# Kernel optimization log

Measured on AMD Instinct MI355X. Metric: run time of the kernel, lower is better.

Reference implementation:

```python
import jax, jax.numpy as jnp
import numpy as np

B, BAG, H, C = 512, 32, 1024, 53
EPS = 1e-8  # torch F.cosine_similarity denominator clamp


def setup_inputs() -> dict:
    key = jax.random.key(0)
    ks = jax.random.split(key, 5)
    return {
        "sent_reps": jax.random.normal(ks[0], (B, BAG, H), jnp.float32),
        "aug_sent_reps": jax.random.normal(ks[1], (B, BAG, H), jnp.float32),
        "rel_table": jax.random.normal(ks[2], (C, H), jnp.float32),
        "cls_w": jax.random.normal(ks[3], (C, H), jnp.float32) * 0.02,
        "cls_b": jnp.zeros((C,), jnp.float32),
        "labels": jax.random.randint(ks[4], (B,), 0, C),
        "temperature": jnp.asarray(0.1, jnp.float32),
    }


def _cl(rep, aug, bag_rep, T):
    # rep, aug: (B, bag, H); bag_rep: (B, H)
    nr = jnp.linalg.norm(rep, axis=-1)        # (B, bag)
    na = jnp.linalg.norm(aug, axis=-1)        # (B, bag)
    nb = jnp.linalg.norm(bag_rep, axis=-1)    # (B,)
    pos_sim = jnp.sum(rep * aug, axis=-1) / jnp.maximum(nr * na, EPS)  # (B, bag)
    pos = jnp.exp(pos_sim / T)
    # pair[c, j, b] = cos(rep[b, j], bag_rep[c])  -- matches torch permute/broadcast chain
    dots = jnp.einsum('bjh,ch->cjb', rep, bag_rep)               # (B, bag, B)
    denom = jnp.maximum(nb[:, None, None] * nr.T[None], EPS)      # (B, bag, B)
    pair = dots / denom
    idx = jnp.arange(rep.shape[0])
    axis_sim = pair[idx, :, idx]                                  # (B, bag): cos(rep[b,j], bag_rep[b])
    neg = jnp.exp(pair / T).sum(axis=2) - jnp.exp(axis_sim / T)   # (B, bag)
    return jnp.mean(-jnp.log(pos / (pos + neg)))


def reference(sent_reps, aug_sent_reps, rel_table, cls_w, cls_b, labels, temperature):
    # Selective attention per bag (scope slices are uniform bags of size BAG -> vectorized)
    rel = rel_table[labels]                                        # (B, H)
    scale = jnp.sqrt(jnp.asarray(H, sent_reps.dtype))
    scores = jnp.einsum('bh,bjh->bj', rel, sent_reps) / scale      # (B, bag)
    alphas = jax.nn.softmax(scores, axis=-1)
    bag_reps = jnp.einsum('bj,bjh->bh', alphas, sent_reps)         # (B, H)
    bag_out = bag_reps @ cls_w.T + cls_b                           # (B, C)  (dropout in eval = identity)
    cl_loss = _cl(sent_reps, aug_sent_reps, bag_reps, temperature)
    return bag_out, cl_loss
```

## Files before the change

kernel.cpp:

```cpp
#include <hip/hip_runtime.h>
#include <hip/hip_bf16.h>


typedef __bf16 bf16x8 __attribute__((ext_vector_type(8)));
typedef float  f32x4  __attribute__((ext_vector_type(4)));

__device__ inline float wsum(float v) {
    #pragma unroll
    for (int off = 32; off > 0; off >>= 1) v += __shfl_xor(v, off, 64);
    return v;
}

__device__ inline void gll16(const void* g, void* l) {
    __builtin_amdgcn_global_load_lds((const __attribute__((address_space(1))) void*)g,
                                     (__attribute__((address_space(3))) void*)l, 16, 0, 0);
}

__global__ __launch_bounds__(256) void k0_cvt(const float* __restrict__ w, __bf16* __restrict__ wb)
{
    int i = blockIdx.x * 256 + threadIdx.x;
    wb[i] = (i < 53 * 1024) ? (__bf16)w[i] : (__bf16)0.0f;
}

__global__ __launch_bounds__(1024) void k1_bag(
    const float* __restrict__ sent, const float* __restrict__ rel_table,
    const int* __restrict__ labels, float* __restrict__ bag,
    __bf16* __restrict__ bagb, float* __restrict__ nb)
{
    const int b = blockIdx.x, t = threadIdx.x;
    const int lane = t & 63, wave = t >> 6;
    __shared__ float red[32 * 16];
    __shared__ float alphas[32];
    __shared__ float r2[16];

    const float relh = rel_table[(size_t)labels[b] * 1024 + t];
    const float* s = sent + (size_t)b * 32 * 1024;
    float v[32];
    #pragma unroll
    for (int j = 0; j < 32; j++) v[j] = s[j * 1024 + t];

    #pragma unroll
    for (int j = 0; j < 32; j++) {
        float p = wsum(relh * v[j]);
        if (lane == 0) red[j * 16 + wave] = p;
    }
    __syncthreads();

    if (wave == 0) {
        float sj = 0.0f;
        if (lane < 32) {
            #pragma unroll
            for (int w = 0; w < 16; w++) sj += red[lane * 16 + w];
            sj *= (1.0f / 32.0f);
        }
        float m = sj;
        #pragma unroll
        for (int off = 16; off > 0; off >>= 1) m = fmaxf(m, __shfl_xor(m, off, 32));
        float e = __expf(sj - m);
        float sum = e;
        #pragma unroll
        for (int off = 16; off > 0; off >>= 1) sum += __shfl_xor(sum, off, 32);
        if (lane < 32) alphas[lane] = e / sum;
    }
    __syncthreads();

    float bg = 0.0f;
    #pragma unroll
    for (int j = 0; j < 32; j++) bg += alphas[j] * v[j];
    bag[(size_t)b * 1024 + t] = bg;
    bagb[(size_t)b * 1024 + t] = (__bf16)bg;

    float q = wsum(bg * bg);
    if (lane == 0) r2[wave] = q;
    __syncthreads();
    if (t == 0) {
        float s2 = 0.0f;
        #pragma unroll
        for (int w = 0; w < 16; w++) s2 += r2[w];
        nb[b] = sqrtf(s2);
    }
}

__global__ __launch_bounds__(256) void k2_norms(
    const float* __restrict__ sent, const float* __restrict__ aug,
    __bf16* __restrict__ repb, float* __restrict__ nr, float* __restrict__ pos_sim)
{
    const int r = blockIdx.x;
    const int t = threadIdx.x;
    const float* rp = sent + (size_t)r * 1024;
    const float* ap = aug + (size_t)r * 1024;
    float sr = 0.f, sa = 0.f, sd = 0.f;
    #pragma unroll
    for (int i = 0; i < 4; i++) {
        int h = t + i * 256;
        float x = rp[h], y = ap[h];
        sr += x * x; sa += y * y; sd += x * y;
        repb[(size_t)r * 1024 + h] = (__bf16)x;
    }
    sr = wsum(sr); sa = wsum(sa); sd = wsum(sd);
    __shared__ float red[4 * 3];
    const int lane = t & 63, wave = t >> 6;
    if (lane == 0) { red[wave * 3] = sr; red[wave * 3 + 1] = sa; red[wave * 3 + 2] = sd; }
    __syncthreads();
    if (t == 0) {
        float S = 0.f, A = 0.f, D = 0.f;
        #pragma unroll
        for (int w = 0; w < 4; w++) { S += red[w * 3]; A += red[w * 3 + 1]; D += red[w * 3 + 2]; }
        float nrv = sqrtf(S), nav = sqrtf(A);
        nr[r] = nrv;
        pos_sim[r] = D / fmaxf(nrv * nav, 1e-8f);
    }
}

__global__ __launch_bounds__(256) void k3m(
    const __bf16* __restrict__ bagb, const __bf16* __restrict__ cwb,
    const float* __restrict__ bias, float* __restrict__ out)
{
    __shared__ __align__(16) __bf16 Al[64 * 40];
    __shared__ __align__(16) __bf16 Bl[64 * 40];
    const int r0 = blockIdx.x * 64;
    const int t = threadIdx.x, lane = t & 63, w = t >> 6;
    const int m = lane & 15, quad = lane >> 4;
    f32x4 acc[4] = {};
    const int lrow = t >> 2, lk = (t & 3) * 8;

    for (int k0 = 0; k0 < 1024; k0 += 32) {
        __syncthreads();
        *(f32x4*)(&Al[lrow * 40 + lk]) = *(const f32x4*)(&bagb[(size_t)(r0 + lrow) * 1024 + k0 + lk]);
        *(f32x4*)(&Bl[lrow * 40 + lk]) = *(const f32x4*)(&cwb[(size_t)lrow * 1024 + k0 + lk]);
        __syncthreads();
        bf16x8 a = *(const bf16x8*)(&Al[(w * 16 + m) * 40 + quad * 8]);
        #pragma unroll
        for (int n = 0; n < 4; n++) {
            bf16x8 bf = *(const bf16x8*)(&Bl[(n * 16 + m) * 40 + quad * 8]);
            acc[n] = __builtin_amdgcn_mfma_f32_16x16x32_bf16(a, bf, acc[n], 0, 0, 0);
        }
    }
    #pragma unroll
    for (int n = 0; n < 4; n++) {
        const int c = n * 16 + m;
        if (c < 53) {
            #pragma unroll
            for (int i = 0; i < 4; i++) {
                const int r = r0 + w * 16 + quad * 4 + i;
                out[(size_t)r * 53 + c] = acc[n][i] + bias[c];
            }
        }
    }
}

__global__ __launch_bounds__(256) void k4_gemm(
    const __bf16* __restrict__ repb, const __bf16* __restrict__ bagb,
    const float* __restrict__ nr, const float* __restrict__ nb,
    const float* __restrict__ temp, float* __restrict__ E)
{
    __shared__ __align__(16) __bf16 Al[128 * 32];
    __shared__ __align__(16) __bf16 Bl[128 * 32];
    const int cb = blockIdx.x, rb = blockIdx.y;
    const int r0 = rb * 128, c0 = cb * 128;
    const int t = threadIdx.x, lane = t & 63, w = t >> 6;
    const int m = lane & 15, quad = lane >> 4;
    const int wr0 = (w & 1) * 64, wc0 = (w >> 1) * 64;

    f32x4 acc[4][4] = {};

    const int i0 = t * 8, i1 = 2048 + t * 8;
    const int row0 = i0 >> 5, kk0 = i0 & 31;
    const int row1 = i1 >> 5, kk1 = i1 & 31;
    const __bf16* gA0 = repb + (size_t)(r0 + row0) * 1024 + kk0;
    const __bf16* gA1 = repb + (size_t)(r0 + row1) * 1024 + kk1;
    const __bf16* gB0 = bagb + (size_t)(c0 + row0) * 1024 + kk0;
    const __bf16* gB1 = bagb + (size_t)(c0 + row1) * 1024 + kk1;

    for (int k0 = 0; k0 < 1024; k0 += 32) {
        __syncthreads();
        gll16(gA0 + k0, Al + i0);
        gll16(gA1 + k0, Al + i1);
        gll16(gB0 + k0, Bl + i0);
        gll16(gB1 + k0, Bl + i1);
        __syncthreads();
        bf16x8 a[4], bf[4];
        #pragma unroll
        for (int i = 0; i < 4; i++) a[i]  = *(const bf16x8*)(&Al[(wr0 + i * 16 + m) * 32 + quad * 8]);
        #pragma unroll
        for (int n = 0; n < 4; n++) bf[n] = *(const bf16x8*)(&Bl[(wc0 + n * 16 + m) * 32 + quad * 8]);
        #pragma unroll
        for (int i = 0; i < 4; i++)
            #pragma unroll
            for (int n = 0; n < 4; n++)
                acc[i][n] = __builtin_amdgcn_mfma_f32_16x16x32_bf16(a[i], bf[n], acc[i][n], 0, 0, 0);
    }

    const float invT = 1.0f / *temp;
    float nrv[16];
    #pragma unroll
    for (int i = 0; i < 4; i++)
        #pragma unroll
        for (int g = 0; g < 4; g++)
            nrv[i * 4 + g] = nr[r0 + wr0 + i * 16 + quad * 4 + g];
    #pragma unroll
    for (int n = 0; n < 4; n++) {
        const int c = c0 + wc0 + n * 16 + m;
        const float nbv = nb[c];
        #pragma unroll
        for (int i = 0; i < 4; i++) {
            #pragma unroll
            for (int g = 0; g < 4; g++) {
                const int r = r0 + wr0 + i * 16 + quad * 4 + g;
                float pair = acc[i][n][g] / fmaxf(nbv * nrv[i * 4 + g], 1e-8f);
                E[(size_t)r * 512 + c] = __expf(pair * invT);
            }
        }
    }
}

__global__ __launch_bounds__(256) void k5_neg(
    const float* __restrict__ E, const float* __restrict__ pos_sim,
    const float* __restrict__ temp, float* __restrict__ bsums)
{
    const int ct = blockIdx.x & 7, j = blockIdx.x >> 3;
    const int t = threadIdx.x, lane = t & 63, w = t >> 6;
    const int c = ct * 64 + lane;
    __shared__ float red[4][64];

    float s = 0.f;
    const float* base = E + (size_t)j * 512 + c;
    #pragma unroll 8
    for (int b = w * 128; b < w * 128 + 128; b++)
        s += base[(size_t)b * 32 * 512];
    red[w][lane] = s;
    __syncthreads();

    if (t < 64) {
        const int cc = ct * 64 + t;
        float S = red[0][t] + red[1][t] + red[2][t] + red[3][t];
        S -= E[(size_t)((cc << 5) + j) * 512 + cc];
        const float invT = 1.0f / *temp;
        const float lp = pos_sim[(cc << 5) + j] * invT;
        float term = logf(__expf(lp) + S) - lp;
        term = wsum(term);
        if (t == 0) bsums[blockIdx.x] = term;
    }
}

__global__ __launch_bounds__(256) void k6_final(const float* __restrict__ bsums, float* __restrict__ loss)
{
    const int t = threadIdx.x;
    float v = bsums[t];
    v = wsum(v);
    __shared__ float r[4];
    if ((t & 63) == 0) r[t >> 6] = v;
    __syncthreads();
    if (t == 0) *loss = (r[0] + r[1] + r[2] + r[3]) * (1.0f / 16384.0f);
}

extern "C" void kernel_launch(void* const* d_in, const int* in_sizes, int n_in,
                              void* d_out, int out_size, void* d_ws, size_t ws_size,
                              hipStream_t stream)
{
    const float* sent = (const float*)d_in[0];
    const float* aug  = (const float*)d_in[1];
    const float* rel  = (const float*)d_in[2];
    const float* clsw = (const float*)d_in[3];
    const float* clsb = (const float*)d_in[4];
    const int*   lab  = (const int*)d_in[5];
    const float* temp = (const float*)d_in[6];
    float* out = (float*)d_out;

    char* ws = (char*)d_ws;
    float*  bag   = (float*)(ws);
    __bf16* bagb  = (__bf16*)(ws + (2u << 20));
    float*  nb    = (float*)(ws + (3u << 20));
    float*  nr    = (float*)(ws + (3u << 20) + 65536);
    float*  pos   = (float*)(ws + (3u << 20) + 2 * 65536);
    __bf16* cwb   = (__bf16*)(ws + (3u << 20) + 3 * 65536);
    __bf16* repb  = (__bf16*)(ws + (4u << 20));
    float*  E     = (float*)(ws + (36u << 20));
    float*  bsums = (float*)(ws + (68u << 20));

    k0_cvt  <<<256, 256, 0, stream>>>(clsw, cwb);
    k1_bag  <<<512, 1024, 0, stream>>>(sent, rel, lab, bag, bagb, nb);
    k2_norms<<<16384, 256, 0, stream>>>(sent, aug, repb, nr, pos);
    k3m     <<<8, 256, 0, stream>>>(bagb, cwb, clsb, out);
    k4_gemm <<<dim3(4, 128), 256, 0, stream>>>(repb, bagb, nr, nb, temp, E);
    k5_neg  <<<256, 256, 0, stream>>>(E, pos, temp, bsums);
    k6_final<<<1, 256, 0, stream>>>(bsums, out + 27136);
}
```

Baseline: 229.6 us.

## Fuse bag and norm kernels, store exp matrix in bf16, remap GEMM blocks to XCDs

Merges the attention-pooling kernel and the per-row norm kernel so sent_reps is read once, with the aug dot products and norms computed in the same pass. The unused fp32 bag output is dropped. The 16384x512 exp matrix E is stored as bf16 instead of fp32, halving its write and read traffic, at some cost in precision of the negative sums. Blocks of the similarity GEMM are remapped so that blocks sharing a row tile land on the same XCD, and the classifier GEMM now loads tiles with direct global-to-LDS loads.

```diff
diff --git a/kernel.cpp b/kernel.cpp
--- a/kernel.cpp
+++ b/kernel.cpp
@@ -22,27 +22,40 @@
     wb[i] = (i < 53 * 1024) ? (__bf16)w[i] : (__bf16)0.0f;
 }
 
-__global__ __launch_bounds__(1024) void k1_bag(
-    const float* __restrict__ sent, const float* __restrict__ rel_table,
-    const int* __restrict__ labels, float* __restrict__ bag,
-    __bf16* __restrict__ bagb, float* __restrict__ nb)
+__global__ __launch_bounds__(1024) void k12(
+    const float* __restrict__ sent, const float* __restrict__ aug,
+    const float* __restrict__ rel_table, const int* __restrict__ labels,
+    __bf16* __restrict__ bagb, float* __restrict__ nb,
+    __bf16* __restrict__ repb, float* __restrict__ nr, float* __restrict__ pos_sim)
 {
     const int b = blockIdx.x, t = threadIdx.x;
     const int lane = t & 63, wave = t >> 6;
-    __shared__ float red[32 * 16];
+    __shared__ float redS[32 * 16];
+    __shared__ float redR[32 * 16];
+    __shared__ float redA[32 * 16];
+    __shared__ float redD[32 * 16];
     __shared__ float alphas[32];
     __shared__ float r2[16];
 
     const float relh = rel_table[(size_t)labels[b] * 1024 + t];
-    const float* s = sent + (size_t)b * 32 * 1024;
+    const float* s  = sent + (size_t)b * 32 * 1024;
+    const float* ag = aug  + (size_t)b * 32 * 1024;
     float v[32];
     #pragma unroll
     for (int j = 0; j < 32; j++) v[j] = s[j * 1024 + t];
 
     #pragma unroll
     for (int j = 0; j < 32; j++) {
-        float p = wsum(relh * v[j]);
-        if (lane == 0) red[j * 16 + wave] = p;
+        float y = ag[j * 1024 + t];
+        float p  = wsum(relh * v[j]);
+        float sr = wsum(v[j] * v[j]);
+        float sa = wsum(y * y);
+        float sd = wsum(v[j] * y);
+        if (lane == 0) {
+            redS[j * 16 + wave] = p;  redR[j * 16 + wave] = sr;
+            redA[j * 16 + wave] = sa; redD[j * 16 + wave] = sd;
+        }
+        repb[(size_t)(b * 32 + j) * 1024 + t] = (__bf16)v[j];
     }
     __syncthreads();
 
@@ -50,7 +63,7 @@
         float sj = 0.0f;
         if (lane < 32) {
             #pragma unroll
-            for (int w = 0; w < 16; w++) sj += red[lane * 16 + w];
+            for (int w = 0; w < 16; w++) sj += redS[lane * 16 + w];
             sj *= (1.0f / 32.0f);
         }
         float m = sj;
@@ -61,13 +74,22 @@
         #pragma unroll
         for (int off = 16; off > 0; off >>= 1) sum += __shfl_xor(sum, off, 32);
         if (lane < 32) alphas[lane] = e / sum;
+    } else if (wave == 1 && lane < 32) {
+        const int j = lane;
+        float R = 0.f, A = 0.f, D = 0.f;
+        #pragma unroll
+        for (int w = 0; w < 16; w++) {
+            R += redR[j * 16 + w]; A += redA[j * 16 + w]; D += redD[j * 16 + w];
+        }
+        float nrv = sqrtf(R), nav = sqrtf(A);
+        nr[b * 32 + j] = nrv;
+        pos_sim[b * 32 + j] = D / fmaxf(nrv * nav, 1e-8f);
     }
     __syncthreads();
 
     float bg = 0.0f;
     #pragma unroll
     for (int j = 0; j < 32; j++) bg += alphas[j] * v[j];
-    bag[(size_t)b * 1024 + t] = bg;
     bagb[(size_t)b * 1024 + t] = (__bf16)bg;
 
     float q = wsum(bg * bg);
@@ -78,37 +100,6 @@
         #pragma unroll
         for (int w = 0; w < 16; w++) s2 += r2[w];
         nb[b] = sqrtf(s2);
-    }
-}
-
-__global__ __launch_bounds__(256) void k2_norms(
-    const float* __restrict__ sent, const float* __restrict__ aug,
-    __bf16* __restrict__ repb, float* __restrict__ nr, float* __restrict__ pos_sim)
-{
-    const int r = blockIdx.x;
-    const int t = threadIdx.x;
-    const float* rp = sent + (size_t)r * 1024;
-    const float* ap = aug + (size_t)r * 1024;
-    float sr = 0.f, sa = 0.f, sd = 0.f;
-    #pragma unroll
-    for (int i = 0; i < 4; i++) {
-        int h = t + i * 256;
-        float x = rp[h], y = ap[h];
-        sr += x * x; sa += y * y; sd += x * y;
-        repb[(size_t)r * 1024 + h] = (__bf16)x;
-    }
-    sr = wsum(sr); sa = wsum(sa); sd = wsum(sd);
-    __shared__ float red[4 * 3];
-    const int lane = t & 63, wave = t >> 6;
-    if (lane == 0) { red[wave * 3] = sr; red[wave * 3 + 1] = sa; red[wave * 3 + 2] = sd; }
-    __syncthreads();
-    if (t == 0) {
-        float S = 0.f, A = 0.f, D = 0.f;
-        #pragma unroll
-        for (int w = 0; w < 4; w++) { S += red[w * 3]; A += red[w * 3 + 1]; D += red[w * 3 + 2]; }
-        float nrv = sqrtf(S), nav = sqrtf(A);
-        nr[r] = nrv;
-        pos_sim[r] = D / fmaxf(nrv * nav, 1e-8f);
     }
 }
 
@@ -116,23 +107,27 @@
     const __bf16* __restrict__ bagb, const __bf16* __restrict__ cwb,
     const float* __restrict__ bias, float* __restrict__ out)
 {
-    __shared__ __align__(16) __bf16 Al[64 * 40];
-    __shared__ __align__(16) __bf16 Bl[64 * 40];
+    __shared__ __align__(16) __bf16 Al[64 * 32];
+    __shared__ __align__(16) __bf16 Bl[64 * 32];
     const int r0 = blockIdx.x * 64;
     const int t = threadIdx.x, lane = t & 63, w = t >> 6;
     const int m = lane & 15, quad = lane >> 4;
     f32x4 acc[4] = {};
-    const int lrow = t >> 2, lk = (t & 3) * 8;
+
+    const int i0 = t * 8;
+    const int row0 = i0 >> 5, kk0 = i0 & 31;
+    const __bf16* gA = bagb + (size_t)(r0 + row0) * 1024 + kk0;
+    const __bf16* gB = cwb + (size_t)row0 * 1024 + kk0;
 
     for (int k0 = 0; k0 < 1024; k0 += 32) {
         __syncthreads();
-        *(f32x4*)(&Al[lrow * 40 + lk]) = *(const f32x4*)(&bagb[(size_t)(r0 + lrow) * 1024 + k0 + lk]);
-        *(f32x4*)(&Bl[lrow * 40 + lk]) = *(const f32x4*)(&cwb[(size_t)lrow * 1024 + k0 + lk]);
-        __syncthreads();
-        bf16x8 a = *(const bf16x8*)(&Al[(w * 16 + m) * 40 + quad * 8]);
+        gll16(gA + k0, Al + i0);
+        gll16(gB + k0, Bl + i0);
+        __syncthreads();
+        bf16x8 a = *(const bf16x8*)(&Al[(w * 16 + m) * 32 + quad * 8]);
         #pragma unroll
         for (int n = 0; n < 4; n++) {
-            bf16x8 bf = *(const bf16x8*)(&Bl[(n * 16 + m) * 40 + quad * 8]);
+            bf16x8 bf = *(const bf16x8*)(&Bl[(n * 16 + m) * 32 + quad * 8]);
             acc[n] = __builtin_amdgcn_mfma_f32_16x16x32_bf16(a, bf, acc[n], 0, 0, 0);
         }
     }
@@ -152,11 +147,13 @@
 __global__ __launch_bounds__(256) void k4_gemm(
     const __bf16* __restrict__ repb, const __bf16* __restrict__ bagb,
     const float* __restrict__ nr, const float* __restrict__ nb,
-    const float* __restrict__ temp, float* __restrict__ E)
+    const float* __restrict__ temp, __bf16* __restrict__ E)
 {
     __shared__ __align__(16) __bf16 Al[128 * 32];
     __shared__ __align__(16) __bf16 Bl[128 * 32];
-    const int cb = blockIdx.x, rb = blockIdx.y;
+    const int bid = blockIdx.x;
+    const int xcd = bid & 7, slot = bid >> 3;
+    const int cb = slot & 3, rb = (slot >> 2) * 8 + xcd;
     const int r0 = rb * 128, c0 = cb * 128;
     const int t = threadIdx.x, lane = t & 63, w = t >> 6;
     const int m = lane & 15, quad = lane >> 4;
@@ -208,14 +205,14 @@
             for (int g = 0; g < 4; g++) {
                 const int r = r0 + wr0 + i * 16 + quad * 4 + g;
                 float pair = acc[i][n][g] / fmaxf(nbv * nrv[i * 4 + g], 1e-8f);
-                E[(size_t)r * 512 + c] = __expf(pair * invT);
+                E[(size_t)r * 512 + c] = (__bf16)__expf(pair * invT);
             }
         }
     }
 }
 
 __global__ __launch_bounds__(256) void k5_neg(
-    const float* __restrict__ E, const float* __restrict__ pos_sim,
+    const __bf16* __restrict__ E, const float* __restrict__ pos_sim,
     const float* __restrict__ temp, float* __restrict__ bsums)
 {
     const int ct = blockIdx.x & 7, j = blockIdx.x >> 3;
@@ -224,17 +221,17 @@
     __shared__ float red[4][64];
 
     float s = 0.f;
-    const float* base = E + (size_t)j * 512 + c;
+    const __bf16* base = E + (size_t)j * 512 + c;
     #pragma unroll 8
     for (int b = w * 128; b < w * 128 + 128; b++)
-        s += base[(size_t)b * 32 * 512];
+        s += (float)base[(size_t)b * 16384];
     red[w][lane] = s;
     __syncthreads();
 
     if (t < 64) {
         const int cc = ct * 64 + t;
         float S = red[0][t] + red[1][t] + red[2][t] + red[3][t];
-        S -= E[(size_t)((cc << 5) + j) * 512 + cc];
+        S -= (float)E[(size_t)((cc << 5) + j) * 512 + cc];
         const float invT = 1.0f / *temp;
         const float lp = pos_sim[(cc << 5) + j] * invT;
         float term = logf(__expf(lp) + S) - lp;
@@ -268,21 +265,19 @@
     float* out = (float*)d_out;
 
     char* ws = (char*)d_ws;
-    float*  bag   = (float*)(ws);
-    __bf16* bagb  = (__bf16*)(ws + (2u << 20));
-    float*  nb    = (float*)(ws + (3u << 20));
-    float*  nr    = (float*)(ws + (3u << 20) + 65536);
-    float*  pos   = (float*)(ws + (3u << 20) + 2 * 65536);
-    __bf16* cwb   = (__bf16*)(ws + (3u << 20) + 3 * 65536);
+    __bf16* bagb  = (__bf16*)(ws);
+    float*  nb    = (float*)(ws + (1u << 20));
+    float*  nr    = (float*)(ws + (1u << 20) + 65536);
+    float*  pos   = (float*)(ws + (1u << 20) + 2 * 65536);
+    __bf16* cwb   = (__bf16*)(ws + (1u << 20) + 3 * 65536);
+    float*  bsums = (float*)(ws + (2u << 20));
     __bf16* repb  = (__bf16*)(ws + (4u << 20));
-    float*  E     = (float*)(ws + (36u << 20));
-    float*  bsums = (float*)(ws + (68u << 20));
+    __bf16* E     = (__bf16*)(ws + (36u << 20));
 
     k0_cvt  <<<256, 256, 0, stream>>>(clsw, cwb);
-    k1_bag  <<<512, 1024, 0, stream>>>(sent, rel, lab, bag, bagb, nb);
-    k2_norms<<<16384, 256, 0, stream>>>(sent, aug, repb, nr, pos);
+    k12     <<<512, 1024, 0, stream>>>(sent, aug, rel, lab, bagb, nb, repb, nr, pos);
     k3m     <<<8, 256, 0, stream>>>(bagb, cwb, clsb, out);
-    k4_gemm <<<dim3(4, 128), 256, 0, stream>>>(repb, bagb, nr, nb, temp, E);
+    k4_gemm <<<512, 256, 0, stream>>>(repb, bagb, nr, nb, temp, E);
     k5_neg  <<<256, 256, 0, stream>>>(E, pos, temp, bsums);
     k6_final<<<1, 256, 0, stream>>>(bsums, out + 27136);
 }
```

After: 267.8 us. 1.17x slower.
